# Optimization experiments

Measured on AMD Instinct MI355X. Metric: run time of the kernel, lower is better.

The kernel has to match this reference:

```python
import jax, jax.numpy as jnp
import numpy as np

HIDDEN = 1024
HEADS = 16
N, T1, T2 = 2, 2048, 2048


def setup_inputs() -> dict:
    key = jax.random.key(0)
    k1, k2, k3, k4 = jax.random.split(key, 4)
    q = jax.random.normal(k1, (N, T1, HIDDEN), dtype=jnp.float32)
    encoder_k = jax.random.normal(k2, (N, T2, HIDDEN), dtype=jnp.float32)
    encoder_v = jax.random.normal(k3, (N, T2, HIDDEN), dtype=jnp.float32)
    encoder_attention_mask = jnp.zeros((N, 1, T2, T2), dtype=jnp.float32)
    wo_w = jax.random.normal(k4, (HIDDEN, HIDDEN), dtype=jnp.float32) * (1.0 / np.sqrt(HIDDEN))
    wo_b = jnp.zeros((HIDDEN,), dtype=jnp.float32)
    return {"q": q, "encoder_k": encoder_k, "encoder_v": encoder_v,
            "encoder_attention_mask": encoder_attention_mask,
            "wo_w": wo_w, "wo_b": wo_b}


def _split_heads(x):
    # [N, T, E] -> [N, h, T, d]
    n, t, e = x.shape
    return x.reshape(n, t, HEADS, e // HEADS).transpose(0, 2, 1, 3)


def reference(q, encoder_k, encoder_v, encoder_attention_mask, wo_w, wo_b):
    qh = _split_heads(q)            # [N,h,T1,d]
    kh = _split_heads(encoder_k)    # [N,h,T2,d]
    vh = _split_heads(encoder_v)    # [N,h,T2,d]
    # NOTE: original applies no 1/sqrt(d) scaling
    scores = jnp.einsum('bhqd,bhkd->bhqk', qh, kh) + encoder_attention_mask
    weights = jax.nn.softmax(scores, axis=-1)
    ctx = jnp.einsum('bhqk,bhkd->bhqd', weights, vh)   # [N,h,T1,d]
    ctx = ctx.transpose(0, 2, 1, 3).reshape(q.shape[0], q.shape[1], -1)  # [N,T1,E]
    # wo: Linear (torch: x @ W.T + b) followed by ReLU
    return jax.nn.relu(ctx @ wo_w.T + wo_b)
```

## Files before the change

### kernel.cpp

```cpp
#include <hip/hip_runtime.h>


typedef short short8 __attribute__((ext_vector_type(8)));
typedef short short4v __attribute__((ext_vector_type(4)));
typedef float floatx4 __attribute__((ext_vector_type(4)));

#define HIDDEN 1024
#define HEADS 16
#define NB 2
#define T1 2048
#define T2 2048

#define LOG2E 1.44269504f
#define SHIFT 28.8539004f
#define VS 68

__device__ __forceinline__ float fexp2(float x) {
#if __has_builtin(__builtin_amdgcn_exp2f)
    return __builtin_amdgcn_exp2f(x);
#else
    return __expf(x * 0.69314718056f);
#endif
}

__device__ __forceinline__ unsigned short f2bf(float f) {
    unsigned u = __float_as_uint(f);
    return (unsigned short)((u + 0x7fffu + ((u >> 16) & 1u)) >> 16);
}

__device__ __forceinline__ int pk_hi16(float a, float b) {
    return (int)__builtin_amdgcn_perm(__float_as_uint(b), __float_as_uint(a), 0x07060302u);
}

union S4 { int2 i2; short4v s; };

__global__ void zero_kernel(unsigned* f) {
    if (threadIdx.x == 0) *f = 0u;
}

__global__ void prep_kernel(const float4* __restrict__ ek, const float4* __restrict__ ev,
                            const float4* __restrict__ ww, const float4* __restrict__ mask,
                            ushort4* __restrict__ dst, unsigned* __restrict__ flag) {
    const int NK = NB * T2 * HIDDEN / 4;
    const int NW = HIDDEN * HIDDEN / 4;
    if (blockIdx.y == 0) {
        int i = blockIdx.x * blockDim.x + threadIdx.x;
        int stride = gridDim.x * blockDim.x;
        const int n = 2 * NK + NW;
        for (; i < n; i += stride) {
            float4 v = (i < NK) ? ek[i] : (i < 2 * NK) ? ev[i - NK] : ww[i - 2 * NK];
            ushort4 o;
            o.x = f2bf(v.x); o.y = f2bf(v.y); o.z = f2bf(v.z); o.w = f2bf(v.w);
            dst[i] = o;
        }
    } else {
        const int NM = NB * T2 * T2 / 4;
        int i = blockIdx.x * blockDim.x + threadIdx.x;
        int stride = gridDim.x * blockDim.x;
        float mx = 0.f;
        for (; i < NM; i += stride) {
            float4 v = mask[i];
            mx = fmaxf(mx, fmaxf(fmaxf(fabsf(v.x), fabsf(v.y)), fmaxf(fabsf(v.z), fabsf(v.w))));
        }
        for (int d = 32; d; d >>= 1) mx = fmaxf(mx, __shfl_xor(mx, d));
        if ((threadIdx.x & 63) == 0 && mx > 0.f) atomicMax(flag, __float_as_uint(mx));
    }
}

struct KFrag { short8 f[4][2]; };

__device__ __forceinline__ void load_k(KFrag& k, const short* __restrict__ Kp,
                                       int kc, int l16, int quad) {
#pragma unroll
    for (int kb = 0; kb < 4; ++kb)
#pragma unroll
        for (int ks = 0; ks < 2; ++ks)
            k.f[kb][ks] = *(const short8*)&Kp[((kc + kb * 16 + l16) << 10) + ks * 32 + quad * 8];
}

__device__ __forceinline__ void stage_v(short* __restrict__ buf, const short* __restrict__ Vp,
                                        int kc, int tid) {
#pragma unroll
    for (int it = 0; it < 2; ++it) {
        int i = tid + (it << 8);
        int key = i & 63, dg = i >> 6;
        short8 s = *(const short8*)&Vp[((kc + key) << 10) + (dg << 3)];
#pragma unroll
        for (int j = 0; j < 8; ++j) buf[(dg * 8 + j) * VS + key] = s[j];
    }
}

__device__ __forceinline__ void do_chunk(
        const KFrag& kf, const short* __restrict__ cur,
        const short8 (&qf)[2][2], floatx4 (&o_acc)[2][4], floatx4 (&o_l)[2],
        const float* __restrict__ mbase, int kc, bool use_mask,
        int quad, int l16, short4v ones)
{
    short4v vfrag[4][4];
#pragma unroll
    for (int kb = 0; kb < 4; ++kb)
#pragma unroll
        for (int cb = 0; cb < 4; ++cb)
            vfrag[kb][cb] = *(const short4v*)&cur[(cb * 16 + l16) * VS + kb * 16 + quad * 4];

#pragma unroll
    for (int rb = 0; rb < 2; ++rb) {
        floatx4 st[4];
#pragma unroll
        for (int kb = 0; kb < 4; ++kb) {
            floatx4 a = (floatx4){-SHIFT, -SHIFT, -SHIFT, -SHIFT};
            a = __builtin_amdgcn_mfma_f32_16x16x32_bf16(kf.f[kb][0], qf[rb][0], a, 0, 0, 0);
            a = __builtin_amdgcn_mfma_f32_16x16x32_bf16(kf.f[kb][1], qf[rb][1], a, 0, 0, 0);
            st[kb] = a;
        }
        if (use_mask) {
            const float* mrow = mbase + (long)(rb * 16 + l16) * T2 + kc;
#pragma unroll
            for (int kb = 0; kb < 4; ++kb)
#pragma unroll
                for (int r = 0; r < 4; ++r)
                    st[kb][r] += mrow[kb * 16 + quad * 4 + r] * LOG2E;
        }
        short4v pf[4];
#pragma unroll
        for (int kb = 0; kb < 4; ++kb) {
            float p0 = fexp2(st[kb][0]);
            float p1 = fexp2(st[kb][1]);
            float p2 = fexp2(st[kb][2]);
            float p3 = fexp2(st[kb][3]);
            S4 u; u.i2 = make_int2(pk_hi16(p0, p1), pk_hi16(p2, p3));
            pf[kb] = u.s;
        }
#pragma unroll
        for (int kb = 0; kb < 4; ++kb) {
            o_l[rb] = __builtin_amdgcn_mfma_f32_16x16x16bf16_1k(ones, pf[kb], o_l[rb], 0, 0, 0);
#pragma unroll
            for (int cb = 0; cb < 4; ++cb)
                o_acc[rb][cb] = __builtin_amdgcn_mfma_f32_16x16x16bf16_1k(
                    vfrag[kb][cb], pf[kb], o_acc[rb][cb], 0, 0, 0);
        }
    }
}

__global__ __launch_bounds__(256) void attn_kernel(
        const float* __restrict__ q,
        const short* __restrict__ Kb,
        const short* __restrict__ Vb,
        const float* __restrict__ mask,
        const unsigned* __restrict__ flagp,
        short* __restrict__ ctx)
{
    __shared__ short lV[2][64 * VS];

    const int tid = threadIdx.x;
    const int wave = tid >> 6;
    const int lane = tid & 63;
    const int quad = lane >> 4;
    const int l16 = lane & 15;

    const int b = blockIdx.z;
    const int h = blockIdx.y;
    const int q0 = blockIdx.x * 128;

    const bool use_mask = (*flagp != 0u);
    const float* mbase = mask + ((long)(b * T2) + q0 + wave * 32) * T2;

    short8 qf[2][2];
#pragma unroll
    for (int rb = 0; rb < 2; ++rb) {
#pragma unroll
        for (int ks = 0; ks < 2; ++ks) {
            const float* qp = q + (((b * T1) + q0 + wave * 32 + rb * 16 + l16) << 10)
                                + (h << 6) + ks * 32 + quad * 8;
            float4 v0 = *(const float4*)qp;
            float4 v1 = *(const float4*)(qp + 4);
            short8 s;
            s[0] = (short)f2bf(v0.x * LOG2E); s[1] = (short)f2bf(v0.y * LOG2E);
            s[2] = (short)f2bf(v0.z * LOG2E); s[3] = (short)f2bf(v0.w * LOG2E);
            s[4] = (short)f2bf(v1.x * LOG2E); s[5] = (short)f2bf(v1.y * LOG2E);
            s[6] = (short)f2bf(v1.z * LOG2E); s[7] = (short)f2bf(v1.w * LOG2E);
            qf[rb][ks] = s;
        }
    }

    floatx4 o_acc[2][4], o_l[2];
#pragma unroll
    for (int rb = 0; rb < 2; ++rb) {
        o_l[rb] = (floatx4){0.f, 0.f, 0.f, 0.f};
#pragma unroll
        for (int cb = 0; cb < 4; ++cb) o_acc[rb][cb] = (floatx4){0.f, 0.f, 0.f, 0.f};
    }
    short4v ones;
#pragma unroll
    for (int j = 0; j < 4; ++j) ones[j] = (short)0x3F80;

    const short* Kp = Kb + ((b * T2) << 10) + (h << 6);
    const short* Vp = Vb + ((b * T2) << 10) + (h << 6);

    KFrag kf0, kf1;
    load_k(kf0, Kp, 0, l16, quad);
    stage_v(lV[0], Vp, 0, tid);
    __syncthreads();

    for (int ic = 0; ic < T2 / 64; ic += 2) {
        stage_v(lV[1], Vp, (ic + 1) << 6, tid);
        load_k(kf1, Kp, (ic + 1) << 6, l16, quad);
        do_chunk(kf0, lV[0], qf, o_acc, o_l, mbase, ic << 6, use_mask, quad, l16, ones);
        __syncthreads();
        if (ic + 2 < T2 / 64) {
            stage_v(lV[0], Vp, (ic + 2) << 6, tid);
            load_k(kf0, Kp, (ic + 2) << 6, l16, quad);
        }
        do_chunk(kf1, lV[1], qf, o_acc, o_l, mbase, (ic + 1) << 6, use_mask, quad, l16, ones);
        __syncthreads();
    }

#pragma unroll
    for (int rb = 0; rb < 2; ++rb) {
        float rinv = 1.0f / o_l[rb][0];
        int qrow = q0 + wave * 32 + rb * 16 + l16;
#pragma unroll
        for (int cb = 0; cb < 4; ++cb) {
            short4v o;
#pragma unroll
            for (int r = 0; r < 4; ++r) o[r] = (short)f2bf(o_acc[rb][cb][r] * rinv);
            *(short4v*)&ctx[((b * T1 + qrow) << 10) + (h << 6) + cb * 16 + quad * 4] = o;
        }
    }
}

__global__ __launch_bounds__(256) void proj_kernel(
        const short* __restrict__ Cb,
        const short* __restrict__ Wb,
        const float* __restrict__ bias,
        float* __restrict__ out)
{
    __shared__ short lA[64 * 72];
    __shared__ short lB[128 * 72];

    const int tid = threadIdx.x;
    const int wave = tid >> 6;
    const int lane = tid & 63;
    const int quad = lane >> 4;
    const int l16 = lane & 15;
    const int wm = wave >> 1, wn = wave & 1;
    const int bm = blockIdx.x, bn = blockIdx.y;

    floatx4 acc[2][4];
#pragma unroll
    for (int i = 0; i < 2; ++i)
#pragma unroll
        for (int j = 0; j < 4; ++j) acc[i][j] = (floatx4){0.f, 0.f, 0.f, 0.f};

    for (int kt = 0; kt < 1024; kt += 64) {
#pragma unroll
        for (int it = 0; it < 2; ++it) {
            int i = tid + it * 256;
            int row = i >> 3, c = i & 7;
            *(short8*)&lA[row * 72 + c * 8] =
                *(const short8*)&Cb[((bm * 64 + row) << 10) + kt + c * 8];
        }
#pragma unroll
        for (int it = 0; it < 4; ++it) {
            int i = tid + it * 256;
            int row = i >> 3, c = i & 7;
            *(short8*)&lB[row * 72 + c * 8] =
                *(const short8*)&Wb[((bn * 128 + row) << 10) + kt + c * 8];
        }
        __syncthreads();
#pragma unroll
        for (int ks = 0; ks < 2; ++ks) {
            short8 af[2], bf[4];
#pragma unroll
            for (int i = 0; i < 2; ++i)
                af[i] = *(const short8*)&lA[(wm * 32 + i * 16 + l16) * 72 + ks * 32 + quad * 8];
#pragma unroll
            for (int j = 0; j < 4; ++j)
                bf[j] = *(const short8*)&lB[(wn * 64 + j * 16 + l16) * 72 + ks * 32 + quad * 8];
#pragma unroll
            for (int i = 0; i < 2; ++i)
#pragma unroll
                for (int j = 0; j < 4; ++j)
                    acc[i][j] = __builtin_amdgcn_mfma_f32_16x16x32_bf16(af[i], bf[j], acc[i][j], 0, 0, 0);
        }
        __syncthreads();
    }

    float bv[4];
#pragma unroll
    for (int j = 0; j < 4; ++j) bv[j] = bias[bn * 128 + wn * 64 + j * 16 + l16];

#pragma unroll
    for (int i = 0; i < 2; ++i)
#pragma unroll
        for (int j = 0; j < 4; ++j)
#pragma unroll
            for (int r = 0; r < 4; ++r) {
                int row = bm * 64 + wm * 32 + i * 16 + quad * 4 + r;
                int col = bn * 128 + wn * 64 + j * 16 + l16;
                float v = acc[i][j][r] + bv[j];
                out[(row << 10) + col] = fmaxf(v, 0.f);
            }
}

extern "C" void kernel_launch(void* const* d_in, const int* in_sizes, int n_in,
                              void* d_out, int out_size, void* d_ws, size_t ws_size,
                              hipStream_t stream) {
    const float* q    = (const float*)d_in[0];
    const float* ek   = (const float*)d_in[1];
    const float* ev   = (const float*)d_in[2];
    const float* mask = (const float*)d_in[3];
    const float* wo_w = (const float*)d_in[4];
    const float* wo_b = (const float*)d_in[5];
    float* out = (float*)d_out;

    char* ws = (char*)d_ws;
    unsigned* flag = (unsigned*)ws;
    short* Kb = (short*)(ws + 4096);
    short* Vb = Kb + (NB * T2 * HIDDEN);
    short* Wb = Vb + (NB * T2 * HIDDEN);
    short* Cb = Wb + (HIDDEN * HIDDEN);

    zero_kernel<<<1, 64, 0, stream>>>(flag);
    prep_kernel<<<dim3(512, 2), 256, 0, stream>>>(
        (const float4*)ek, (const float4*)ev, (const float4*)wo_w, (const float4*)mask,
        (ushort4*)Kb, flag);
    attn_kernel<<<dim3(T1 / 128, HEADS, NB), 256, 0, stream>>>(q, Kb, Vb, mask, flag, Cb);
    proj_kernel<<<dim3(64, 8), 256, 0, stream>>>(Cb, Wb, wo_b, out);
}
```

Baseline: 259.8 us.

## Pre-transpose K/V into head-major layouts and drop LDS staging in attention and projection

The prep kernel now writes K in head-major order and V transposed per head (via an LDS transpose in a third grid slice), so attention waves load K and V fragments straight from global memory without LDS staging or barriers. Each attention wave handles 16 query rows instead of 32, with smaller blocks and a 4-blocks-per-CU launch bound. The projection GEMM also drops LDS tiling and reads fragments directly from global with smaller 64x64 tiles. The aim is to remove LDS transpose traffic and syncs and raise occupancy, at the cost of less K/V reuse per wave and more reliance on the cache for global reads.

```diff
diff --git a/kernel.cpp b/kernel.cpp
--- a/kernel.cpp
+++ b/kernel.cpp
@@ -13,7 +13,6 @@
 
 #define LOG2E 1.44269504f
 #define SHIFT 28.8539004f
-#define VS 68
 
 __device__ __forceinline__ float fexp2(float x) {
 #if __has_builtin(__builtin_amdgcn_exp2f)
@@ -38,88 +37,150 @@
     if (threadIdx.x == 0) *f = 0u;
 }
 
-__global__ void prep_kernel(const float4* __restrict__ ek, const float4* __restrict__ ev,
-                            const float4* __restrict__ ww, const float4* __restrict__ mask,
-                            ushort4* __restrict__ dst, unsigned* __restrict__ flag) {
-    const int NK = NB * T2 * HIDDEN / 4;
-    const int NW = HIDDEN * HIDDEN / 4;
+__global__ __launch_bounds__(256) void prep_kernel(
+        const float4* __restrict__ ek, const float4* __restrict__ ev,
+        const float4* __restrict__ ww, const float4* __restrict__ mask,
+        ushort4* __restrict__ Khm,
+        ushort4* __restrict__ Wb,
+        short*   __restrict__ Vt,
+        unsigned* __restrict__ flag)
+{
+    __shared__ short lds[64 * 68];
+    const int t = threadIdx.x;
     if (blockIdx.y == 0) {
-        int i = blockIdx.x * blockDim.x + threadIdx.x;
-        int stride = gridDim.x * blockDim.x;
-        const int n = 2 * NK + NW;
+        const int NKf4 = NB * T2 * HIDDEN / 4;
+        const int n = NKf4 + HIDDEN * HIDDEN / 4;
+        int i = blockIdx.x * 256 + t;
+        const int stride = gridDim.x * 256;
         for (; i < n; i += stride) {
-            float4 v = (i < NK) ? ek[i] : (i < 2 * NK) ? ev[i - NK] : ww[i - 2 * NK];
-            ushort4 o;
-            o.x = f2bf(v.x); o.y = f2bf(v.y); o.z = f2bf(v.z); o.w = f2bf(v.w);
-            dst[i] = o;
-        }
-    } else {
+            if (i < NKf4) {
+                float4 v = ek[i];
+                ushort4 o;
+                o.x = f2bf(v.x); o.y = f2bf(v.y); o.z = f2bf(v.z); o.w = f2bf(v.w);
+                int b = i >> 19, r = i & 524287;
+                int key = r >> 8, c4 = r & 255;
+                int h = c4 >> 4, d4 = c4 & 15;
+                Khm[(((b * 16 + h) * 2048 + key) << 4) + d4] = o;
+            } else {
+                float4 v = ww[i - NKf4];
+                ushort4 o;
+                o.x = f2bf(v.x); o.y = f2bf(v.y); o.z = f2bf(v.z); o.w = f2bf(v.w);
+                Wb[i - NKf4] = o;
+            }
+        }
+    } else if (blockIdx.y == 1) {
         const int NM = NB * T2 * T2 / 4;
-        int i = blockIdx.x * blockDim.x + threadIdx.x;
-        int stride = gridDim.x * blockDim.x;
+        int i = blockIdx.x * 256 + t;
+        const int stride = gridDim.x * 256;
         float mx = 0.f;
         for (; i < NM; i += stride) {
             float4 v = mask[i];
             mx = fmaxf(mx, fmaxf(fmaxf(fabsf(v.x), fabsf(v.y)), fmaxf(fabsf(v.z), fabsf(v.w))));
         }
         for (int d = 32; d; d >>= 1) mx = fmaxf(mx, __shfl_xor(mx, d));
-        if ((threadIdx.x & 63) == 0 && mx > 0.f) atomicMax(flag, __float_as_uint(mx));
-    }
-}
-
-struct KFrag { short8 f[4][2]; };
-
-__device__ __forceinline__ void load_k(KFrag& k, const short* __restrict__ Kp,
-                                       int kc, int l16, int quad) {
-#pragma unroll
-    for (int kb = 0; kb < 4; ++kb)
-#pragma unroll
-        for (int ks = 0; ks < 2; ++ks)
-            k.f[kb][ks] = *(const short8*)&Kp[((kc + kb * 16 + l16) << 10) + ks * 32 + quad * 8];
-}
-
-__device__ __forceinline__ void stage_v(short* __restrict__ buf, const short* __restrict__ Vp,
-                                        int kc, int tid) {
-#pragma unroll
-    for (int it = 0; it < 2; ++it) {
-        int i = tid + (it << 8);
-        int key = i & 63, dg = i >> 6;
-        short8 s = *(const short8*)&Vp[((kc + key) << 10) + (dg << 3)];
-#pragma unroll
-        for (int j = 0; j < 8; ++j) buf[(dg * 8 + j) * VS + key] = s[j];
-    }
-}
-
-__device__ __forceinline__ void do_chunk(
-        const KFrag& kf, const short* __restrict__ cur,
-        const short8 (&qf)[2][2], floatx4 (&o_acc)[2][4], floatx4 (&o_l)[2],
-        const float* __restrict__ mbase, int kc, bool use_mask,
-        int quad, int l16, short4v ones)
+        if ((t & 63) == 0 && mx > 0.f) atomicMax(flag, __float_as_uint(mx));
+    } else {
+        const int x = blockIdx.x;
+        const int kt = x & 31, h = (x >> 5) & 15, b = x >> 9;
+        const int key0 = kt * 64;
+#pragma unroll
+        for (int it = 0; it < 4; ++it) {
+            int idx = t + it * 256;
+            int key = idx >> 4, f4 = idx & 15;
+            float4 v = ev[(b * T2 + key0 + key) * 256 + h * 16 + f4];
+            short4v o;
+            o[0] = (short)f2bf(v.x); o[1] = (short)f2bf(v.y);
+            o[2] = (short)f2bf(v.z); o[3] = (short)f2bf(v.w);
+            *(short4v*)&lds[key * 68 + f4 * 4] = o;
+        }
+        __syncthreads();
+        const int dim = t >> 2, kq = t & 3;
+        short8 s0, s1;
+#pragma unroll
+        for (int kk = 0; kk < 8; ++kk) s0[kk] = lds[(kq * 16 + kk) * 68 + dim];
+#pragma unroll
+        for (int kk = 0; kk < 8; ++kk) s1[kk] = lds[(kq * 16 + 8 + kk) * 68 + dim];
+        short* Vr = Vt + ((b * 16 + h) * 64 + dim) * T2 + key0 + kq * 16;
+        *(short8*)&Vr[0] = s0;
+        *(short8*)&Vr[8] = s1;
+    }
+}
+
+__global__ __launch_bounds__(256, 4) void attn_kernel(
+        const float* __restrict__ q,
+        const short* __restrict__ Khm,
+        const short* __restrict__ Vt,
+        const float* __restrict__ mask,
+        const unsigned* __restrict__ flagp,
+        short* __restrict__ ctx)
 {
-    short4v vfrag[4][4];
-#pragma unroll
-    for (int kb = 0; kb < 4; ++kb)
-#pragma unroll
-        for (int cb = 0; cb < 4; ++cb)
-            vfrag[kb][cb] = *(const short4v*)&cur[(cb * 16 + l16) * VS + kb * 16 + quad * 4];
-
-#pragma unroll
-    for (int rb = 0; rb < 2; ++rb) {
+    const int tid = threadIdx.x;
+    const int wave = tid >> 6;
+    const int lane = tid & 63;
+    const int quad = lane >> 4;
+    const int l16 = lane & 15;
+
+    const int b = blockIdx.z;
+    const int h = blockIdx.y;
+    const int qrow = blockIdx.x * 64 + wave * 16 + l16;
+
+    const bool use_mask = (*flagp != 0u);
+
+    short8 qf[2];
+#pragma unroll
+    for (int ks = 0; ks < 2; ++ks) {
+        const float* qp = q + (((b * T1) + qrow) << 10) + (h << 6) + ks * 32 + quad * 8;
+        float4 v0 = *(const float4*)qp;
+        float4 v1 = *(const float4*)(qp + 4);
+        short8 s;
+        s[0] = (short)f2bf(v0.x * LOG2E); s[1] = (short)f2bf(v0.y * LOG2E);
+        s[2] = (short)f2bf(v0.z * LOG2E); s[3] = (short)f2bf(v0.w * LOG2E);
+        s[4] = (short)f2bf(v1.x * LOG2E); s[5] = (short)f2bf(v1.y * LOG2E);
+        s[6] = (short)f2bf(v1.z * LOG2E); s[7] = (short)f2bf(v1.w * LOG2E);
+        qf[ks] = s;
+    }
+
+    floatx4 o_acc[4], o_l;
+#pragma unroll
+    for (int cb = 0; cb < 4; ++cb) o_acc[cb] = (floatx4){0.f, 0.f, 0.f, 0.f};
+    o_l = (floatx4){0.f, 0.f, 0.f, 0.f};
+    short4v ones;
+#pragma unroll
+    for (int j = 0; j < 4; ++j) ones[j] = (short)0x3F80;
+
+    const short* Kp = Khm + ((b * 16 + h) * 2048) * 64;
+    const short* Vp = Vt + ((b * 16 + h) * 64) * 2048;
+    const float* mrow = mask + ((long)(b * T2) + qrow) * T2;
+
+    for (int kc = 0; kc < T2; kc += 64) {
+        short8 kf[4][2];
+#pragma unroll
+        for (int kb = 0; kb < 4; ++kb)
+#pragma unroll
+            for (int ks = 0; ks < 2; ++ks)
+                kf[kb][ks] = *(const short8*)&Kp[(kc + kb * 16 + l16) * 64 + ks * 32 + quad * 8];
+
+        short4v vf[4][4];
+#pragma unroll
+        for (int kb = 0; kb < 4; ++kb)
+#pragma unroll
+            for (int cb = 0; cb < 4; ++cb)
+                vf[kb][cb] = *(const short4v*)&Vp[(cb * 16 + l16) * 2048 + kc + kb * 16 + quad * 4];
+
         floatx4 st[4];
 #pragma unroll
         for (int kb = 0; kb < 4; ++kb) {
             floatx4 a = (floatx4){-SHIFT, -SHIFT, -SHIFT, -SHIFT};
-            a = __builtin_amdgcn_mfma_f32_16x16x32_bf16(kf.f[kb][0], qf[rb][0], a, 0, 0, 0);
-            a = __builtin_amdgcn_mfma_f32_16x16x32_bf16(kf.f[kb][1], qf[rb][1], a, 0, 0, 0);
+            a = __builtin_amdgcn_mfma_f32_16x16x32_bf16(kf[kb][0], qf[0], a, 0, 0, 0);
+            a = __builtin_amdgcn_mfma_f32_16x16x32_bf16(kf[kb][1], qf[1], a, 0, 0, 0);
             st[kb] = a;
         }
         if (use_mask) {
-            const float* mrow = mbase + (long)(rb * 16 + l16) * T2 + kc;
 #pragma unroll
             for (int kb = 0; kb < 4; ++kb)
 #pragma unroll
                 for (int r = 0; r < 4; ++r)
-                    st[kb][r] += mrow[kb * 16 + quad * 4 + r] * LOG2E;
+                    st[kb][r] += mrow[kc + kb * 16 + quad * 4 + r] * LOG2E;
         }
         short4v pf[4];
 #pragma unroll
@@ -133,173 +194,74 @@
         }
 #pragma unroll
         for (int kb = 0; kb < 4; ++kb) {
-            o_l[rb] = __builtin_amdgcn_mfma_f32_16x16x16bf16_1k(ones, pf[kb], o_l[rb], 0, 0, 0);
+            o_l = __builtin_amdgcn_mfma_f32_16x16x16bf16_1k(ones, pf[kb], o_l, 0, 0, 0);
 #pragma unroll
             for (int cb = 0; cb < 4; ++cb)
-                o_acc[rb][cb] = __builtin_amdgcn_mfma_f32_16x16x16bf16_1k(
-                    vfrag[kb][cb], pf[kb], o_acc[rb][cb], 0, 0, 0);
-        }
-    }
-}
-
-__global__ __launch_bounds__(256) void attn_kernel(
-        const float* __restrict__ q,
-        const short* __restrict__ Kb,
-        const short* __restrict__ Vb,
-        const float* __restrict__ mask,
-        const unsigned* __restrict__ flagp,
-        short* __restrict__ ctx)
-{
-    __shared__ short lV[2][64 * VS];
-
-    const int tid = threadIdx.x;
-    const int wave = tid >> 6;
-    const int lane = tid & 63;
-    const int quad = lane >> 4;
-    const int l16 = lane & 15;
-
-    const int b = blockIdx.z;
-    const int h = blockIdx.y;
-    const int q0 = blockIdx.x * 128;
-
-    const bool use_mask = (*flagp != 0u);
-    const float* mbase = mask + ((long)(b * T2) + q0 + wave * 32) * T2;
-
-    short8 qf[2][2];
-#pragma unroll
-    for (int rb = 0; rb < 2; ++rb) {
-#pragma unroll
-        for (int ks = 0; ks < 2; ++ks) {
-            const float* qp = q + (((b * T1) + q0 + wave * 32 + rb * 16 + l16) << 10)
-                                + (h << 6) + ks * 32 + quad * 8;
-            float4 v0 = *(const float4*)qp;
-            float4 v1 = *(const float4*)(qp + 4);
-            short8 s;
-            s[0] = (short)f2bf(v0.x * LOG2E); s[1] = (short)f2bf(v0.y * LOG2E);
-            s[2] = (short)f2bf(v0.z * LOG2E); s[3] = (short)f2bf(v0.w * LOG2E);
-            s[4] = (short)f2bf(v1.x * LOG2E); s[5] = (short)f2bf(v1.y * LOG2E);
-            s[6] = (short)f2bf(v1.z * LOG2E); s[7] = (short)f2bf(v1.w * LOG2E);
-            qf[rb][ks] = s;
-        }
-    }
-
-    floatx4 o_acc[2][4], o_l[2];
-#pragma unroll
-    for (int rb = 0; rb < 2; ++rb) {
-        o_l[rb] = (floatx4){0.f, 0.f, 0.f, 0.f};
-#pragma unroll
-        for (int cb = 0; cb < 4; ++cb) o_acc[rb][cb] = (floatx4){0.f, 0.f, 0.f, 0.f};
-    }
-    short4v ones;
-#pragma unroll
-    for (int j = 0; j < 4; ++j) ones[j] = (short)0x3F80;
-
-    const short* Kp = Kb + ((b * T2) << 10) + (h << 6);
-    const short* Vp = Vb + ((b * T2) << 10) + (h << 6);
-
-    KFrag kf0, kf1;
-    load_k(kf0, Kp, 0, l16, quad);
-    stage_v(lV[0], Vp, 0, tid);
-    __syncthreads();
-
-    for (int ic = 0; ic < T2 / 64; ic += 2) {
-        stage_v(lV[1], Vp, (ic + 1) << 6, tid);
-        load_k(kf1, Kp, (ic + 1) << 6, l16, quad);
-        do_chunk(kf0, lV[0], qf, o_acc, o_l, mbase, ic << 6, use_mask, quad, l16, ones);
-        __syncthreads();
-        if (ic + 2 < T2 / 64) {
-            stage_v(lV[0], Vp, (ic + 2) << 6, tid);
-            load_k(kf0, Kp, (ic + 2) << 6, l16, quad);
-        }
-        do_chunk(kf1, lV[1], qf, o_acc, o_l, mbase, (ic + 1) << 6, use_mask, quad, l16, ones);
-        __syncthreads();
-    }
-
-#pragma unroll
-    for (int rb = 0; rb < 2; ++rb) {
-        float rinv = 1.0f / o_l[rb][0];
-        int qrow = q0 + wave * 32 + rb * 16 + l16;
-#pragma unroll
-        for (int cb = 0; cb < 4; ++cb) {
-            short4v o;
-#pragma unroll
-            for (int r = 0; r < 4; ++r) o[r] = (short)f2bf(o_acc[rb][cb][r] * rinv);
-            *(short4v*)&ctx[((b * T1 + qrow) << 10) + (h << 6) + cb * 16 + quad * 4] = o;
-        }
-    }
-}
-
-__global__ __launch_bounds__(256) void proj_kernel(
+                o_acc[cb] = __builtin_amdgcn_mfma_f32_16x16x16bf16_1k(
+                    vf[kb][cb], pf[kb], o_acc[cb], 0, 0, 0);
+        }
+    }
+
+    const float rinv = 1.0f / o_l[0];
+#pragma unroll
+    for (int cb = 0; cb < 4; ++cb) {
+        short4v o;
+#pragma unroll
+        for (int r = 0; r < 4; ++r) o[r] = (short)f2bf(o_acc[cb][r] * rinv);
+        *(short4v*)&ctx[((b * T1 + qrow) << 10) + (h << 6) + cb * 16 + quad * 4] = o;
+    }
+}
+
+__global__ __launch_bounds__(256, 4) void proj_kernel(
         const short* __restrict__ Cb,
         const short* __restrict__ Wb,
         const float* __restrict__ bias,
         float* __restrict__ out)
 {
-    __shared__ short lA[64 * 72];
-    __shared__ short lB[128 * 72];
-
     const int tid = threadIdx.x;
     const int wave = tid >> 6;
     const int lane = tid & 63;
     const int quad = lane >> 4;
     const int l16 = lane & 15;
     const int wm = wave >> 1, wn = wave & 1;
-    const int bm = blockIdx.x, bn = blockIdx.y;
-
-    floatx4 acc[2][4];
+    const int m0 = blockIdx.x * 64 + wm * 32;
+    const int n0 = blockIdx.y * 64 + wn * 32;
+
+    const short* Arow = Cb + (m0 + l16) * 1024 + quad * 8;
+    const short* Brow = Wb + (n0 + l16) * 1024 + quad * 8;
+
+    floatx4 acc[2][2];
 #pragma unroll
     for (int i = 0; i < 2; ++i)
 #pragma unroll
-        for (int j = 0; j < 4; ++j) acc[i][j] = (floatx4){0.f, 0.f, 0.f, 0.f};
-
-    for (int kt = 0; kt < 1024; kt += 64) {
-#pragma unroll
-        for (int it = 0; it < 2; ++it) {
-            int i = tid + it * 256;
-            int row = i >> 3, c = i & 7;
-            *(short8*)&lA[row * 72 + c * 8] =
-                *(const short8*)&Cb[((bm * 64 + row) << 10) + kt + c * 8];
-        }
-#pragma unroll
-        for (int it = 0; it < 4; ++it) {
-            int i = tid + it * 256;
-            int row = i >> 3, c = i & 7;
-            *(short8*)&lB[row * 72 + c * 8] =
-                *(const short8*)&Wb[((bn * 128 + row) << 10) + kt + c * 8];
-        }
-        __syncthreads();
-#pragma unroll
-        for (int ks = 0; ks < 2; ++ks) {
-            short8 af[2], bf[4];
-#pragma unroll
-            for (int i = 0; i < 2; ++i)
-                af[i] = *(const short8*)&lA[(wm * 32 + i * 16 + l16) * 72 + ks * 32 + quad * 8];
-#pragma unroll
-            for (int j = 0; j < 4; ++j)
-                bf[j] = *(const short8*)&lB[(wn * 64 + j * 16 + l16) * 72 + ks * 32 + quad * 8];
-#pragma unroll
-            for (int i = 0; i < 2; ++i)
-#pragma unroll
-                for (int j = 0; j < 4; ++j)
-                    acc[i][j] = __builtin_amdgcn_mfma_f32_16x16x32_bf16(af[i], bf[j], acc[i][j], 0, 0, 0);
-        }
-        __syncthreads();
-    }
-
-    float bv[4];
-#pragma unroll
-    for (int j = 0; j < 4; ++j) bv[j] = bias[bn * 128 + wn * 64 + j * 16 + l16];
+        for (int j = 0; j < 2; ++j) acc[i][j] = (floatx4){0.f, 0.f, 0.f, 0.f};
+
+    for (int kt = 0; kt < 1024; kt += 32) {
+        short8 af[2], bf[2];
+#pragma unroll
+        for (int i = 0; i < 2; ++i) af[i] = *(const short8*)&Arow[i * 16 * 1024 + kt];
+#pragma unroll
+        for (int j = 0; j < 2; ++j) bf[j] = *(const short8*)&Brow[j * 16 * 1024 + kt];
+#pragma unroll
+        for (int i = 0; i < 2; ++i)
+#pragma unroll
+            for (int j = 0; j < 2; ++j)
+                acc[i][j] = __builtin_amdgcn_mfma_f32_16x16x32_bf16(af[i], bf[j], acc[i][j], 0, 0, 0);
+    }
+
+    float bv[2];
+#pragma unroll
+    for (int j = 0; j < 2; ++j) bv[j] = bias[n0 + j * 16 + l16];
 
 #pragma unroll
     for (int i = 0; i < 2; ++i)
 #pragma unroll
-        for (int j = 0; j < 4; ++j)
+        for (int j = 0; j < 2; ++j)
 #pragma unroll
             for (int r = 0; r < 4; ++r) {
-                int row = bm * 64 + wm * 32 + i * 16 + quad * 4 + r;
-                int col = bn * 128 + wn * 64 + j * 16 + l16;
-                float v = acc[i][j][r] + bv[j];
-                out[(row << 10) + col] = fmaxf(v, 0.f);
+                int row = m0 + i * 16 + quad * 4 + r;
+                int col = n0 + j * 16 + l16;
+                out[(row << 10) + col] = fmaxf(acc[i][j][r] + bv[j], 0.f);
             }
 }
 
@@ -316,15 +278,15 @@
 
     char* ws = (char*)d_ws;
     unsigned* flag = (unsigned*)ws;
-    short* Kb = (short*)(ws + 4096);
-    short* Vb = Kb + (NB * T2 * HIDDEN);
-    short* Wb = Vb + (NB * T2 * HIDDEN);
-    short* Cb = Wb + (HIDDEN * HIDDEN);
+    short* Khm = (short*)(ws + 4096);
+    short* Wb  = Khm + (NB * T2 * HIDDEN);
+    short* Vt  = Wb + (HIDDEN * HIDDEN);
+    short* Cb  = Vt + (NB * T2 * HIDDEN);
 
     zero_kernel<<<1, 64, 0, stream>>>(flag);
-    prep_kernel<<<dim3(512, 2), 256, 0, stream>>>(
+    prep_kernel<<<dim3(1024, 3), 256, 0, stream>>>(
         (const float4*)ek, (const float4*)ev, (const float4*)wo_w, (const float4*)mask,
-        (ushort4*)Kb, flag);
-    attn_kernel<<<dim3(T1 / 128, HEADS, NB), 256, 0, stream>>>(q, Kb, Vb, mask, flag, Cb);
-    proj_kernel<<<dim3(64, 8), 256, 0, stream>>>(Cb, Wb, wo_b, out);
-}
+        (ushort4*)Khm, (ushort4*)Wb, Vt, flag);
+    attn_kernel<<<dim3(T1 / 64, HEADS, NB), 256, 0, stream>>>(q, Khm, Vt, mask, flag, Cb);
+    proj_kernel<<<dim3(64, 16), 256, 0, stream>>>(Cb, Wb, wo_b, out);
+}
```

Result: slower. 519.3 us (+99.8%).
